# Kernel optimization log

Measured on AMD Instinct MI355X. Metric: run time of the kernel, lower is better.

The kernel has to match this reference:

```python
import jax, jax.numpy as jnp
import numpy as np
import math

N, D, F, G = 8192, 512, 2048, 102
GAMMA = 0.5
NEG = -1e9


def setup_inputs() -> dict:
    key = jax.random.key(0)
    ks = jax.random.split(key, 32)
    x = jax.random.normal(ks[0], (N, D), dtype=jnp.float32)
    real_edge_mask = jax.random.bernoulli(ks[1], 0.9, (N, N))  # True = masked (non-edge)
    fake_edge_mask = jax.random.bernoulli(ks[2], 0.1, (N, N))
    # per-row distinct sorted drop indices over gene_list = arange(D)
    r = jax.random.uniform(ks[3], (N, D))
    drop_idx = jnp.sort(jnp.argsort(r, axis=1)[:, :G], axis=1).astype(jnp.int32)
    s = 1.0 / math.sqrt(D)
    def W(k, m, n):
        return jax.random.normal(k, (m, n), dtype=jnp.float32) * s
    inp = {
        'x': x, 'drop_idx': drop_idx,
        'real_edge_mask': real_edge_mask, 'fake_edge_mask': fake_edge_mask,
        'enc_Wq_r': W(ks[4], D, D), 'enc_Wk_r': W(ks[5], D, D),
        'enc_Wq_f': W(ks[6], D, D), 'enc_Wk_f': W(ks[7], D, D), 'enc_Wv': W(ks[8], D, D),
        'dec_Wq_r': W(ks[9], D, D), 'dec_Wk_r': W(ks[10], D, D),
        'dec_Wq_f': W(ks[11], D, D), 'dec_Wk_f': W(ks[12], D, D), 'dec_Wv': W(ks[13], D, D),
        'ff_W1': W(ks[14], D, F), 'ff_b1': jnp.zeros((F,), jnp.float32),
        'ff_W2': W(ks[15], F, D), 'ff_b2': jnp.zeros((D,), jnp.float32),
        'ln1_g': jnp.ones((D,), jnp.float32), 'ln1_b': jnp.zeros((D,), jnp.float32),
        'ln2_g': jnp.ones((D,), jnp.float32), 'ln2_b': jnp.zeros((D,), jnp.float32),
        'ln3_g': jnp.ones((D,), jnp.float32), 'ln3_b': jnp.zeros((D,), jnp.float32),
        'head_W': W(ks[16], D, D), 'head_b': jnp.zeros((D,), jnp.float32),
    }
    return inp


def layer_norm(h, g, b, eps=1e-5):
    mu = h.mean(-1, keepdims=True)
    var = ((h - mu) ** 2).mean(-1, keepdims=True)
    return (h - mu) * jax.lax.rsqrt(var + eps) * g + b


def spatial_attention(h, Wq_r, Wk_r, Wq_f, Wk_f, Wv, rmask, fmask, gamma):
    d = h.shape[-1]
    scale = 1.0 / math.sqrt(d)
    sr = jnp.where(rmask, NEG, (h @ Wq_r) @ (h @ Wk_r).T * scale)  # [N,N]
    sf = jnp.where(fmask, NEG, (h @ Wq_f) @ (h @ Wk_f).T * scale)  # [N,N]
    m = jnp.maximum(sr.max(axis=1, keepdims=True), sf.max(axis=1, keepdims=True))
    scores = (jnp.exp(sr - m) + gamma * jnp.exp(sf - m)) / (1.0 + gamma)
    attn = scores / scores.sum(axis=-1, keepdims=True)
    return attn @ (h @ Wv), attn


def reference(x, drop_idx, real_edge_mask, fake_edge_mask,
              enc_Wq_r, enc_Wk_r, enc_Wq_f, enc_Wk_f, enc_Wv,
              dec_Wq_r, dec_Wk_r, dec_Wq_f, dec_Wk_f, dec_Wv,
              ff_W1, ff_b1, ff_W2, ff_b2,
              ln1_g, ln1_b, ln2_g, ln2_b, ln3_g, ln3_b,
              head_W, head_b):
    rows = jnp.arange(x.shape[0])[:, None]
    drop_x = x.at[rows, drop_idx].set(0.0)
    hidden, _ = spatial_attention(drop_x, enc_Wq_r, enc_Wk_r, enc_Wq_f, enc_Wk_f, enc_Wv,
                                  real_edge_mask, fake_edge_mask, GAMMA)
    hidden = layer_norm(hidden + drop_x, ln1_g, ln1_b)
    ff = jax.nn.gelu(hidden @ ff_W1 + ff_b1, approximate=False) @ ff_W2 + ff_b2
    hidden = layer_norm(hidden + ff, ln2_g, ln2_b)
    recon, _ = spatial_attention(hidden, dec_Wq_r, dec_Wk_r, dec_Wq_f, dec_Wk_f, dec_Wv,
                                 real_edge_mask, fake_edge_mask, GAMMA)
    recon = layer_norm(recon + hidden, ln3_g, ln3_b)
    h = recon @ head_W + head_b
    x_init = jnp.take_along_axis(x, drop_idx, axis=1)    # [N,G]
    x_recon = jnp.take_along_axis(h, drop_idx, axis=1)   # [N,G]
    return x_init, x_recon
```

## Files before the change

### kernel.cpp

```cpp
#include <hip/hip_runtime.h>
#include <cstdint>
#include <cstddef>


typedef unsigned short u16;
typedef __bf16 bf16x8 __attribute__((ext_vector_type(8)));
typedef float f32x4 __attribute__((ext_vector_type(4)));

#define GAMMA_C 0.5f
#define SCALE_C 0.04419417382415922f
#define NG      (8192 * 102)
#define SLAB    ((size_t)8192 * 512)

__device__ __forceinline__ float b2f(u16 u) {
  union { unsigned int i; float f; } c; c.i = ((unsigned int)u) << 16; return c.f;
}
__device__ __forceinline__ u16 f2b(float f) {
  union { float f; unsigned int i; } c; c.f = f;
  unsigned int u = c.i + 0x7FFFu + ((c.i >> 16) & 1u);
  return (u16)(u >> 16);
}
__device__ __forceinline__ float gelu_exact(float x) {
  return 0.5f * x * (1.0f + erff(x * 0.70710678118654752f));
}
__device__ __forceinline__ int idx_at(const void* p, int i, int i64) {
  return i64 ? (int)((const long long*)p)[i] : ((const int*)p)[i];
}
__device__ __forceinline__ float fl_at(const void* p, size_t i, int f32m) {
  return f32m ? ((const float*)p)[i] : b2f(((const u16*)p)[i]);
}
__device__ __forceinline__ void mask8(const void* m, size_t base, int f, bool o[8]) {
  if (f == 1) {
    unsigned long long v = *(const unsigned long long*)((const unsigned char*)m + base);
#pragma unroll
    for (int e = 0; e < 8; ++e) o[e] = ((v >> (8 * e)) & 0xFF) != 0;
  } else if (f == 0) {
    const uint4 a = *(const uint4*)((const int*)m + base);
    const uint4 b = *(const uint4*)((const int*)m + base + 4);
    o[0] = a.x; o[1] = a.y; o[2] = a.z; o[3] = a.w;
    o[4] = b.x; o[5] = b.y; o[6] = b.z; o[7] = b.w;
  } else if (f == 2) {
    const uint4 v = *(const uint4*)((const u16*)m + base);
    const u16* p = (const u16*)&v;
#pragma unroll
    for (int e = 0; e < 8; ++e) o[e] = p[e] != 0;
  } else {
    const uint4 a = *(const uint4*)((const float*)m + base);
    const uint4 b = *(const uint4*)((const float*)m + base + 4);
    o[0] = a.x; o[1] = a.y; o[2] = a.z; o[3] = a.w;
    o[4] = b.x; o[5] = b.y; o[6] = b.z; o[7] = b.w;
  }
}

#define GLD16(g, l) __builtin_amdgcn_global_load_lds(                         \
    (const __attribute__((address_space(1))) void*)(g),                       \
    (__attribute__((address_space(3))) void*)(l), 16, 0, 0)

__global__ void detect_all(const unsigned char* __restrict__ rmask,
                           const void* __restrict__ xin,
                           const void* __restrict__ idx,
                           int* __restrict__ flags) {
  __shared__ int nz[4];
  __shared__ int mx, bl;
  const int t = threadIdx.x;
  if (t < 4) nz[t] = 0;
  if (t == 0) { mx = 0; bl = 0; }
  __syncthreads();
  int cnt = 0, lm = 0;
  for (int i = t; i < 4096; i += 256) {
    const int v = rmask[i];
    if (v) { ++cnt; if (v > lm) lm = v; }
  }
  if (cnt) atomicAdd(&nz[t & 3], cnt);
  if (lm) atomicMax(&mx, lm);
  int bcnt = 0;
  for (int i = t; i < 2048; i += 256) {
    const u16 u = ((const u16*)xin)[2 * i];
    const int e = (u >> 7) & 0xFF;
    if ((e >= 110 && e <= 141) || u == 0) ++bcnt;
  }
  atomicAdd(&bl, bcnt);
  __syncthreads();
  if (t == 0) {
    int f;
    if (nz[1] == 0 && nz[2] == 0 && nz[3] == 0) f = 0;
    else if (nz[0] == 0 && nz[1] == 0) f = 3;
    else if (mx <= 1) f = 1;
    else f = 2;
    flags[0] = f;
    flags[2] = (bl >= 1536) ? 0 : 1;
    int ok = 1, prev = -1;
    for (int j = 0; j < 102; ++j) {
      const int v = ((const int*)idx)[j];
      if (v <= prev || v < 0 || v >= 512) { ok = 0; break; }
      prev = v;
    }
    flags[1] = ok ? 0 : 1;
  }
}

__global__ void bitmask_prep(const void* __restrict__ mr, const void* __restrict__ mf,
                             unsigned char* __restrict__ bmr, unsigned char* __restrict__ bmf,
                             const int* __restrict__ flags) {
  const int i = blockIdx.x * 256 + threadIdx.x;
  const int f = flags[0];
  bool mk[8];
  mask8(mr, (size_t)i * 8, f, mk);
  unsigned char b = 0;
#pragma unroll
  for (int e = 0; e < 8; ++e) b |= (unsigned char)mk[e] << e;
  bmr[i] = b;
  mask8(mf, (size_t)i * 8, f, mk);
  b = 0;
#pragma unroll
  for (int e = 0; e < 8; ++e) b |= (unsigned char)mk[e] << e;
  bmf[i] = b;
}

struct PtrPack { const void* p[11]; };
__global__ void transpose_cvt_b(PtrPack srcs, u16* __restrict__ out,
                                const int* __restrict__ flags) {
  __shared__ u16 tile[32][33];
  const void* in = srcs.p[blockIdx.z];
  u16* o = out + (size_t)blockIdx.z * 512 * 512;
  const int f32m = flags[2];
  const int c0 = blockIdx.x * 32, r0 = blockIdx.y * 32;
  const int tx = threadIdx.x, ty = threadIdx.y;
  for (int i = ty; i < 32; i += 8) {
    const size_t src = (size_t)(r0 + i) * 512 + (c0 + tx);
    tile[i][tx] = f32m ? f2b(((const float*)in)[src]) : ((const u16*)in)[src];
  }
  __syncthreads();
  for (int i = ty; i < 32; i += 8)
    o[(size_t)(c0 + i) * 512 + (r0 + tx)] = tile[tx][i];
}
__global__ void transpose_cvt(const void* __restrict__ in, u16* __restrict__ out,
                              int R, int C, const int* __restrict__ flags) {
  __shared__ u16 tile[32][33];
  const int f32m = flags[2];
  const int c0 = blockIdx.x * 32, r0 = blockIdx.y * 32;
  const int tx = threadIdx.x, ty = threadIdx.y;
  for (int i = ty; i < 32; i += 8) {
    const size_t src = (size_t)(r0 + i) * C + (c0 + tx);
    tile[i][tx] = f32m ? f2b(((const float*)in)[src]) : ((const u16*)in)[src];
  }
  __syncthreads();
  for (int i = ty; i < 32; i += 8)
    out[(size_t)(c0 + i) * R + (r0 + tx)] = tile[tx][i];
}

__global__ void cvt_to_bf16(const void* __restrict__ in, u16* __restrict__ out,
                            int n, const int* __restrict__ flags) {
  const int i = blockIdx.x * blockDim.x + threadIdx.x;
  if (i < n)
    out[i] = flags[2] ? f2b(((const float*)in)[i]) : ((const u16*)in)[i];
}
__global__ void zero_f32(float* __restrict__ p, int n) {
  const int i = blockIdx.x * blockDim.x + threadIdx.x;
  if (i < n) p[i] = 0.f;
}
__global__ void zero_drop(u16* __restrict__ dx, const void* __restrict__ idx,
                          const int* __restrict__ flags) {
  const int i = blockIdx.x * blockDim.x + threadIdx.x;
  if (i < NG) {
    const int row = i / 102;
    dx[(size_t)row * 512 + idx_at(idx, i, flags[1])] = 0;
  }
}
__global__ void gather_out_k(const void* __restrict__ x, const u16* __restrict__ hs,
                             const void* __restrict__ hb,
                             const void* __restrict__ idx, void* __restrict__ out,
                             const int* __restrict__ flags) {
  const int i = blockIdx.x * blockDim.x + threadIdx.x;
  if (i < NG) {
    const int row = i / 102;
    const int c = idx_at(idx, i, flags[1]);
    const size_t src = (size_t)row * 512 + c;
    const float hv = b2f(hs[src]) + b2f(hs[src + SLAB]) + fl_at(hb, c, flags[2]);
    if (flags[2]) {
      ((float*)out)[i] = ((const float*)x)[src];
      ((float*)out)[NG + i] = hv;
    } else {
      ((u16*)out)[i] = ((const u16*)x)[src];
      ((u16*)out)[NG + i] = f2b(hv);
    }
  }
}

__global__ __launch_bounds__(256)
void gemm_bt(const u16* __restrict__ A, int lda,
             const u16* __restrict__ Bt, int ldb,
             u16* __restrict__ C, int ldc,
             int K, int mode, const void* __restrict__ bias,
             const int* __restrict__ flags, u16* __restrict__ aux,
             long long slabStride) {
  __shared__ alignas(16) u16 smem[16384];
  u16* As = smem;
  u16* Bs = smem + 8192;
  const int tid = threadIdx.x;
  const int lane = tid & 63, wave = tid >> 6;
  const int l15 = lane & 15, l4 = lane >> 4;
  const int wm = (wave >> 1) << 6, wn = (wave & 1) << 6;
  const int m0 = blockIdx.y << 7, n0 = blockIdx.x << 7;
  const size_t kShift = (size_t)blockIdx.z * (size_t)K;
  C += (size_t)blockIdx.z * (size_t)slabStride;

  f32x4 acc[4][4];
#pragma unroll
  for (int i = 0; i < 4; ++i)
#pragma unroll
    for (int j = 0; j < 4; ++j) acc[i][j] = (f32x4){0.f, 0.f, 0.f, 0.f};

  const int lrow = lane >> 3;
  const int lcg = (lane & 7) ^ lrow;
  const u16* aG = A + kShift + (size_t)(m0 + wave * 8 + lrow) * lda + lcg * 8;
  const u16* bG = Bt + kShift + (size_t)(n0 + wave * 8 + lrow) * ldb + lcg * 8;
  u16* asDst = &As[(wave * 8) * 64];
  u16* bsDst = &Bs[(wave * 8) * 64];
  const int swz = (l15 & 7) << 3;

  for (int k0 = 0; k0 < K; k0 += 64) {
#pragma unroll
    for (int r = 0; r < 4; ++r) {
      GLD16(aG + (size_t)(r * 32) * lda + k0, asDst + r * 32 * 64);
      GLD16(bG + (size_t)(r * 32) * ldb + k0, bsDst + r * 32 * 64);
    }
    __syncthreads();
#pragma unroll
    for (int kk = 0; kk < 2; ++kk) {
      bf16x8 a[4], b[4];
      const int koff = (((kk << 2) + l4) << 3) ^ swz;
#pragma unroll
      for (int i = 0; i < 4; ++i) {
        a[i] = *(const bf16x8*)&As[(wm + (i << 4) + l15) * 64 + koff];
        b[i] = *(const bf16x8*)&Bs[(wn + (i << 4) + l15) * 64 + koff];
      }
#pragma unroll
      for (int i = 0; i < 4; ++i)
#pragma unroll
        for (int j = 0; j < 4; ++j)
          acc[i][j] = __builtin_amdgcn_mfma_f32_16x16x32_bf16(a[i], b[j], acc[i][j], 0, 0, 0);
    }
    __syncthreads();
  }

  const int f32m = flags[2];

  if (mode == 2 && n0 >= 2048) {
#pragma unroll
    for (int i = 0; i < 4; ++i) {
      const int rbase = m0 + wm + (i << 4) + l4 * 4;
#pragma unroll
      for (int j = 0; j < 4; ++j) {
        const int gn = n0 - 2048 + wn + (j << 4) + l15;
        ushort4 pk;
        pk.x = f2b(acc[i][j][0]); pk.y = f2b(acc[i][j][1]);
        pk.z = f2b(acc[i][j][2]); pk.w = f2b(acc[i][j][3]);
        *(ushort4*)&aux[(size_t)gn * 8192 + rbase] = pk;
      }
    }
    return;
  }

#pragma unroll
  for (int i = 0; i < 4; ++i) {
    const int rl0 = wm + (i << 4) + l4 * 4;
#pragma unroll
    for (int j = 0; j < 4; ++j) {
      const int cl = wn + (j << 4) + l15;
      float bv = 0.f;
      if (bias) bv = fl_at(bias, n0 + cl, f32m);
      const int chunk = cl >> 3, within = cl & 7;
#pragma unroll
      for (int r = 0; r < 4; ++r) {
        const int rl = rl0 + r;
        float v = acc[i][j][r] + bv;
        if (mode == 1) v = gelu_exact(v);
        const int wchunk = (chunk & 8) | ((chunk ^ rl) & 7);
        smem[rl * 128 + wchunk * 8 + within] = f2b(v);
      }
    }
  }
  __syncthreads();

  const int r = tid >> 1, h = tid & 1;
  const int grow = m0 + r;
#pragma unroll
  for (int cb = 0; cb < 8; ++cb) {
    const int chunkidx = h * 8 + cb;
    const int rchunk = (chunkidx & 8) | ((chunkidx ^ r) & 7);
    uint4 raw = *(const uint4*)&smem[r * 128 + rchunk * 8];
    *(uint4*)&C[(size_t)grow * ldc + n0 + chunkidx * 8] = raw;
  }
}

__global__ __launch_bounds__(256, 3)
void score_fused(const u16* __restrict__ P,
                 const unsigned char* __restrict__ bmr,
                 const unsigned char* __restrict__ bmf,
                 u16* __restrict__ W, float* __restrict__ lvec) {
  __shared__ alignas(16) u16 stage[16384];
  __shared__ unsigned long long mrs[256], mfs[256];
  const int tid = threadIdx.x;
  const int lane = tid & 63, wave = tid >> 6;
  const int l15 = lane & 15, l4 = lane >> 4;
  const int wm = (wave >> 1) << 6, wn = (wave & 1) << 6;
  const int m0 = blockIdx.y << 7, n0 = blockIdx.x << 7;

  {
    const int r = tid >> 1, hh = tid & 1;
    const size_t mo = (size_t)(m0 + r) * 1024 + (n0 >> 3) + hh * 8;
    mrs[tid] = *(const unsigned long long*)&bmr[mo];
    mfs[tid] = *(const unsigned long long*)&bmf[mo];
  }

  const int lrow = lane >> 3;
  const int lcg = (lane & 7) ^ lrow;
  const int swz = (l15 & 7) << 3;
  u16* asDst = &stage[(wave * 8) * 64];
  u16* bsDst = &stage[8192 + (wave * 8) * 64];

  unsigned int srp[4][4][2];
  f32x4 acc[4][4];

  for (int p = 0; p < 2; ++p) {
#pragma unroll
    for (int i = 0; i < 4; ++i)
#pragma unroll
      for (int j = 0; j < 4; ++j) acc[i][j] = (f32x4){0.f, 0.f, 0.f, 0.f};

    const u16* aG = P + (p ? 1024 : 0) + (size_t)(m0 + wave * 8 + lrow) * 2048 + lcg * 8;
    const u16* bG = P + (p ? 1536 : 512) + (size_t)(n0 + wave * 8 + lrow) * 2048 + lcg * 8;

    for (int k0 = 0; k0 < 512; k0 += 64) {
#pragma unroll
      for (int r = 0; r < 4; ++r) {
        GLD16(aG + (size_t)(r * 32) * 2048 + k0, asDst + r * 32 * 64);
        GLD16(bG + (size_t)(r * 32) * 2048 + k0, bsDst + r * 32 * 64);
      }
      __syncthreads();
#pragma unroll
      for (int kk = 0; kk < 2; ++kk) {
        bf16x8 a[4], b[4];
        const int koff = (((kk << 2) + l4) << 3) ^ swz;
#pragma unroll
        for (int i = 0; i < 4; ++i) {
          a[i] = *(const bf16x8*)&stage[(wm + (i << 4) + l15) * 64 + koff];
          b[i] = *(const bf16x8*)&stage[8192 + (wn + (i << 4) + l15) * 64 + koff];
        }
#pragma unroll
        for (int i = 0; i < 4; ++i)
#pragma unroll
          for (int j = 0; j < 4; ++j)
            acc[i][j] = __builtin_amdgcn_mfma_f32_16x16x32_bf16(a[i], b[j], acc[i][j], 0, 0, 0);
      }
      __syncthreads();
    }

    if (p == 0) {
#pragma unroll
      for (int i = 0; i < 4; ++i)
#pragma unroll
        for (int j = 0; j < 4; ++j) {
          srp[i][j][0] = (unsigned int)f2b(acc[i][j][0] * SCALE_C)
                       | ((unsigned int)f2b(acc[i][j][1] * SCALE_C) << 16);
          srp[i][j][1] = (unsigned int)f2b(acc[i][j][2] * SCALE_C)
                       | ((unsigned int)f2b(acc[i][j][3] * SCALE_C) << 16);
        }
    }
  }

  const int hb = wn >> 6;
#pragma unroll
  for (int i = 0; i < 4; ++i) {
    const int rl0 = wm + (i << 4) + l4 * 4;
#pragma unroll
    for (int r = 0; r < 4; ++r) {
      const int rl = rl0 + r;
      const unsigned long long mr = mrs[rl * 2 + hb];
      const unsigned long long mf = mfs[rl * 2 + hb];
      float rsum = 0.f;
#pragma unroll
      for (int j = 0; j < 4; ++j) {
        const int cl = wn + (j << 4) + l15;
        const int bit = cl & 63;
        const float srv = b2f((u16)(srp[i][j][r >> 1] >> ((r & 1) * 16)));
        const float sfv = acc[i][j][r] * SCALE_C;
        const float wr = ((mr >> bit) & 1) ? 0.f : __expf(srv);
        const float wf = ((mf >> bit) & 1) ? 0.f : __expf(sfv);
        const float w = wr + GAMMA_C * wf;
        rsum += w;
        const int chunk = cl >> 3, within = cl & 7;
        const int wchunk = (chunk & 8) | ((chunk ^ rl) & 7);
        stage[rl * 128 + wchunk * 8 + within] = f2b(w);
      }
      rsum += __shfl_xor(rsum, 1);
      rsum += __shfl_xor(rsum, 2);
      rsum += __shfl_xor(rsum, 4);
      rsum += __shfl_xor(rsum, 8);
      if (l15 == 0) atomicAdd(&lvec[m0 + rl], rsum);
    }
  }
  __syncthreads();

  const int rr = tid >> 1, hh = tid & 1;
  const int grow = m0 + rr;
#pragma unroll
  for (int cb = 0; cb < 8; ++cb) {
    const int chunkidx = hh * 8 + cb;
    const int rchunk = (chunkidx & 8) | ((chunkidx ^ rr) & 7);
    uint4 raw = *(const uint4*)&stage[rr * 128 + rchunk * 8];
    *(uint4*)&W[(size_t)grow * 8192 + n0 + chunkidx * 8] = raw;
  }
}

__global__ __launch_bounds__(512)
void pv_big(const u16* __restrict__ W, const u16* __restrict__ Vt,
            u16* __restrict__ slabs) {
  __shared__ alignas(16) u16 smem[24576];
  u16* As = smem;
  u16* Bs = smem + 8192;
  const int tid = threadIdx.x;
  const int lane = tid & 63, wave = tid >> 6;
  const int l15 = lane & 15, l4 = lane >> 4;
  const int wm = (wave >> 2) << 6;
  const int wn = (wave & 3) << 6;
  const int m0 = blockIdx.y << 7, n0 = blockIdx.x << 8;
  const int kbase = blockIdx.z << 10;
  u16* slab = slabs + (size_t)blockIdx.z * SLAB;

  f32x4 acc[4][4];
#pragma unroll
  for (int i = 0; i < 4; ++i)
#pragma unroll
    for (int j = 0; j < 4; ++j) acc[i][j] = (f32x4){0.f, 0.f, 0.f, 0.f};

  const int lrow = lane >> 3;
  const int lcg = (lane & 7) ^ lrow;
  const u16* aG = W + (size_t)(m0 + wave * 8 + lrow) * 8192 + kbase + lcg * 8;
  const u16* bG = Vt + (size_t)(n0 + wave * 8 + lrow) * 8192 + kbase + lcg * 8;
  u16* asDst = &As[(wave * 8) * 64];
  u16* bsDst = &Bs[(wave * 8) * 64];
  const int swz = (l15 & 7) << 3;

  for (int k0 = 0; k0 < 1024; k0 += 64) {
#pragma unroll
    for (int r = 0; r < 2; ++r)
      GLD16(aG + (size_t)(r * 64) * 8192 + k0, asDst + r * 64 * 64);
#pragma unroll
    for (int r = 0; r < 4; ++r)
      GLD16(bG + (size_t)(r * 64) * 8192 + k0, bsDst + r * 64 * 64);
    __syncthreads();
#pragma unroll
    for (int kk = 0; kk < 2; ++kk) {
      bf16x8 a[4], b[4];
      const int koff = (((kk << 2) + l4) << 3) ^ swz;
#pragma unroll
      for (int i = 0; i < 4; ++i) {
        a[i] = *(const bf16x8*)&As[(wm + (i << 4) + l15) * 64 + koff];
        b[i] = *(const bf16x8*)&Bs[(wn + (i << 4) + l15) * 64 + koff];
      }
#pragma unroll
      for (int i = 0; i < 4; ++i)
#pragma unroll
        for (int j = 0; j < 4; ++j)
          acc[i][j] = __builtin_amdgcn_mfma_f32_16x16x32_bf16(a[i], b[j], acc[i][j], 0, 0, 0);
    }
    __syncthreads();
  }

#pragma unroll
  for (int i = 0; i < 4; ++i) {
    const int rbase = m0 + wm + (i << 4) + l4 * 4;
#pragma unroll
    for (int j = 0; j < 4; ++j) {
      const int gn = n0 + wn + (j << 4) + l15;
      ushort4 pk;
      pk.x = f2b(acc[i][j][0]); pk.y = f2b(acc[i][j][1]);
      pk.z = f2b(acc[i][j][2]); pk.w = f2b(acc[i][j][3]);
      *(ushort4*)&slab[((size_t)(rbase >> 2) * 512 + gn) * 4] = pk;
    }
  }
}

__global__ __launch_bounds__(512)
void pv_ln4(const u16* __restrict__ slabs, const float* __restrict__ lvec,
            const u16* __restrict__ res, const void* __restrict__ g,
            const void* __restrict__ be, u16* __restrict__ out,
            const int* __restrict__ flags) {
  const int gid = blockIdx.x;
  const int col = threadIdx.x;
  const int lane = col & 63, wave = col >> 6;
  const int f32m = flags[2];
  float o[4] = {0.f, 0.f, 0.f, 0.f};
  const size_t base = ((size_t)gid * 512 + col) * 4;
#pragma unroll
  for (int s = 0; s < 8; ++s) {
    const ushort4 v = *(const ushort4*)&slabs[s * SLAB + base];
    o[0] += b2f(v.x); o[1] += b2f(v.y); o[2] += b2f(v.z); o[3] += b2f(v.w);
  }
  float v[4];
#pragma unroll
  for (int q = 0; q < 4; ++q) {
    const int grow = gid * 4 + q;
    v[q] = o[q] / lvec[grow] + b2f(res[(size_t)grow * 512 + col]);
  }
  __shared__ float s1[4][8], s2[4][8];
#pragma unroll
  for (int q = 0; q < 4; ++q) {
    float sm = v[q], sq = v[q] * v[q];
#pragma unroll
    for (int d = 1; d < 64; d <<= 1) {
      sm += __shfl_xor(sm, d);
      sq += __shfl_xor(sq, d);
    }
    if (lane == 0) { s1[q][wave] = sm; s2[q][wave] = sq; }
  }
  __syncthreads();
  const float gv = fl_at(g, col, f32m), bv = fl_at(be, col, f32m);
#pragma unroll
  for (int q = 0; q < 4; ++q) {
    float sm = 0.f, sq = 0.f;
#pragma unroll
    for (int w = 0; w < 8; ++w) { sm += s1[q][w]; sq += s2[q][w]; }
    const float mu = sm * (1.f / 512.f);
    const float var = sq * (1.f / 512.f) - mu * mu;
    const float rs = rsqrtf(var + 1e-5f);
    out[(size_t)(gid * 4 + q) * 512 + col] = f2b((v[q] - mu) * rs * gv + bv);
  }
}

__global__ __launch_bounds__(256)
void ff_ln(const u16* __restrict__ slabs, const void* __restrict__ bias,
           const u16* __restrict__ res, const void* __restrict__ g,
           const void* __restrict__ be, u16* __restrict__ out,
           const int* __restrict__ flags) {
  const int row = blockIdx.x, tid = threadIdx.x;
  const int f32m = flags[2];
  const size_t off = (size_t)row * 512 + tid * 2;
  const float v0 = b2f(slabs[off]) + b2f(slabs[off + SLAB])
                 + fl_at(bias, tid * 2, f32m) + b2f(res[off]);
  const float v1 = b2f(slabs[off + 1]) + b2f(slabs[off + 1 + SLAB])
                 + fl_at(bias, tid * 2 + 1, f32m) + b2f(res[off + 1]);
  __shared__ float r1[256], r2[256];
  r1[tid] = v0 + v1;
  r2[tid] = v0 * v0 + v1 * v1;
  __syncthreads();
  for (int s = 128; s > 0; s >>= 1) {
    if (tid < s) { r1[tid] += r1[tid + s]; r2[tid] += r2[tid + s]; }
    __syncthreads();
  }
  const float mu = r1[0] * (1.f / 512.f);
  const float var = r2[0] * (1.f / 512.f) - mu * mu;
  const float rs = rsqrtf(var + 1e-5f);
  out[off]     = f2b((v0 - mu) * rs * fl_at(g, tid * 2, f32m)     + fl_at(be, tid * 2, f32m));
  out[off + 1] = f2b((v1 - mu) * rs * fl_at(g, tid * 2 + 1, f32m) + fl_at(be, tid * 2 + 1, f32m));
}

extern "C" void kernel_launch(void* const* d_in, const int* in_sizes, int n_in,
                              void* d_out, int out_size, void* d_ws, size_t ws_size,
                              hipStream_t stream) {
  (void)in_sizes; (void)n_in; (void)out_size; (void)ws_size;
  const void* x = d_in[0];
  const void* dropidx = d_in[1];
  const void* rmask = d_in[2];
  const void* fmask = d_in[3];

  char* base = (char*)d_ws;
  size_t cur = 0;
  auto alloc = [&](size_t b) -> void* {
    void* p = base + cur;
    cur += (b + 255) & ~(size_t)255;
    return p;
  };

  int* flags = (int*)alloc(256);
  u16* Wt = (u16*)alloc((size_t)11 * 512 * 512 * 2);
  u16* wff1t = (u16*)alloc((size_t)2048 * 512 * 2);
  u16* wff2t = (u16*)alloc((size_t)512 * 2048 * 2);
  const size_t ND2 = (size_t)8192 * 512 * 2;
  u16* dropx = (u16*)alloc(ND2);
  u16* P = (u16*)alloc((size_t)8192 * 2048 * 2);
  u16* Vt = (u16*)alloc(ND2);
  u16* H1 = (u16*)alloc(ND2);
  u16* H2 = (u16*)alloc(ND2);
  u16* FF1 = (u16*)alloc((size_t)8192 * 2048 * 2);
  unsigned char* bmr = (unsigned char*)alloc((size_t)8192 * 1024);
  unsigned char* bmf = (unsigned char*)alloc((size_t)8192 * 1024);
  float* lvec = (float*)alloc((size_t)8192 * 4);
  u16* slabs = (u16*)alloc((size_t)8 * SLAB * 2);
  u16* Wb = (u16*)alloc((size_t)8192 * 8192 * 2);

  detect_all<<<1, 256, 0, stream>>>((const unsigned char*)rmask, x, dropidx, flags);
  bitmask_prep<<<32768, 256, 0, stream>>>(rmask, fmask, bmr, bmf, flags);

  const dim3 tb(32, 8);
  PtrPack wp;
  for (int i = 0; i < 5; ++i) wp.p[i] = d_in[4 + i];
  for (int i = 0; i < 5; ++i) wp.p[5 + i] = d_in[9 + i];
  wp.p[10] = d_in[24];
  transpose_cvt_b<<<dim3(16, 16, 11), tb, 0, stream>>>(wp, Wt, flags);
  transpose_cvt<<<dim3(64, 16), tb, 0, stream>>>(d_in[14], wff1t, 512, 2048, flags);
  transpose_cvt<<<dim3(16, 64), tb, 0, stream>>>(d_in[16], wff2t, 2048, 512, flags);

  cvt_to_bf16<<<(8192 * 512 + 255) / 256, 256, 0, stream>>>(x, dropx, 8192 * 512, flags);
  zero_drop<<<(NG + 255) / 256, 256, 0, stream>>>(dropx, dropidx, flags);

  auto gemm = [&](const u16* A, int lda, const u16* Bt, int ldb, u16* Cc, int ldc,
                  int M, int Nn, int K, int mode, const void* bias, u16* aux,
                  int zc, long long slabStride) {
    gemm_bt<<<dim3(Nn / 128, M / 128, zc), 256, 0, stream>>>(
        A, lda, Bt, ldb, Cc, ldc, K, mode, bias, flags, aux, slabStride);
  };

  auto attention = [&](const u16* Hin, const u16* Wqkv, const void* lnG,
                       const void* lnB, u16* outLN) {
    zero_f32<<<32, 256, 0, stream>>>(lvec, 8192);
    gemm(Hin, 512, Wqkv, 512, P, 2048, 8192, 2560, 512, 2, nullptr, Vt, 1, 0);
    score_fused<<<dim3(64, 64), 256, 0, stream>>>(P, bmr, bmf, Wb, lvec);
    pv_big<<<dim3(2, 64, 8), 512, 0, stream>>>(Wb, Vt, slabs);
    pv_ln4<<<2048, 512, 0, stream>>>(slabs, lvec, Hin, lnG, lnB, outLN, flags);
  };

  attention(dropx, Wt, d_in[18], d_in[19], H1);
  gemm(H1, 512, wff1t, 512, FF1, 2048, 8192, 2048, 512, 1, d_in[15], nullptr, 1, 0);
  gemm(FF1, 2048, wff2t, 2048, slabs, 512, 8192, 512, 1024, 0, nullptr, nullptr,
       2, (long long)SLAB);
  ff_ln<<<8192, 256, 0, stream>>>(slabs, d_in[17], H1, d_in[20], d_in[21], H2, flags);
  attention(H2, Wt + (size_t)5 * 512 * 512, d_in[22], d_in[23], H1);
  gemm(H1, 512, Wt + (size_t)10 * 512 * 512, 512, slabs, 512, 8192, 512, 256, 0,
       nullptr, nullptr, 2, (long long)SLAB);
  gather_out_k<<<(NG + 255) / 256, 256, 0, stream>>>(x, slabs, d_in[25], dropidx,
                                                     d_out, flags);
}
```

Baseline: 1.446 ms.

## Widen score tile to 128x256 with 512 threads and halve PV split-K

After: 1.506 ms. 1.04x slower.

```diff
diff --git a/kernel.cpp b/kernel.cpp
--- a/kernel.cpp
+++ b/kernel.cpp
@@ -294,24 +294,25 @@
   }
 }
 
-__global__ __launch_bounds__(256, 3)
+__global__ __launch_bounds__(512, 4)
 void score_fused(const u16* __restrict__ P,
                  const unsigned char* __restrict__ bmr,
                  const unsigned char* __restrict__ bmf,
                  u16* __restrict__ W, float* __restrict__ lvec) {
-  __shared__ alignas(16) u16 stage[16384];
-  __shared__ unsigned long long mrs[256], mfs[256];
+  __shared__ alignas(16) u16 stage[32768];
+  __shared__ unsigned long long mrs[128][4], mfs[128][4];
   const int tid = threadIdx.x;
   const int lane = tid & 63, wave = tid >> 6;
   const int l15 = lane & 15, l4 = lane >> 4;
-  const int wm = (wave >> 1) << 6, wn = (wave & 1) << 6;
-  const int m0 = blockIdx.y << 7, n0 = blockIdx.x << 7;
+  const int wm = (wave >> 2) << 6;
+  const int wn = (wave & 3) << 6;
+  const int m0 = blockIdx.y << 7, n0 = blockIdx.x << 8;
 
   {
-    const int r = tid >> 1, hh = tid & 1;
-    const size_t mo = (size_t)(m0 + r) * 1024 + (n0 >> 3) + hh * 8;
-    mrs[tid] = *(const unsigned long long*)&bmr[mo];
-    mfs[tid] = *(const unsigned long long*)&bmf[mo];
+    const int rl = tid >> 2, q = tid & 3;
+    const size_t mo = (size_t)(m0 + rl) * 1024 + (n0 >> 3) + q * 8;
+    mrs[rl][q] = *(const unsigned long long*)&bmr[mo];
+    mfs[rl][q] = *(const unsigned long long*)&bmf[mo];
   }
 
   const int lrow = lane >> 3;
@@ -334,10 +335,11 @@
 
     for (int k0 = 0; k0 < 512; k0 += 64) {
 #pragma unroll
-      for (int r = 0; r < 4; ++r) {
-        GLD16(aG + (size_t)(r * 32) * 2048 + k0, asDst + r * 32 * 64);
-        GLD16(bG + (size_t)(r * 32) * 2048 + k0, bsDst + r * 32 * 64);
-      }
+      for (int r = 0; r < 2; ++r)
+        GLD16(aG + (size_t)(r * 64) * 2048 + k0, asDst + r * 64 * 64);
+#pragma unroll
+      for (int r = 0; r < 4; ++r)
+        GLD16(bG + (size_t)(r * 64) * 2048 + k0, bsDst + r * 64 * 64);
       __syncthreads();
 #pragma unroll
       for (int kk = 0; kk < 2; ++kk) {
@@ -370,29 +372,29 @@
     }
   }
 
-  const int hb = wn >> 6;
+  const int qw = wn >> 6;
 #pragma unroll
   for (int i = 0; i < 4; ++i) {
     const int rl0 = wm + (i << 4) + l4 * 4;
 #pragma unroll
     for (int r = 0; r < 4; ++r) {
       const int rl = rl0 + r;
-      const unsigned long long mr = mrs[rl * 2 + hb];
-      const unsigned long long mf = mfs[rl * 2 + hb];
+      const unsigned long long mr = mrs[rl][qw];
+      const unsigned long long mf = mfs[rl][qw];
       float rsum = 0.f;
 #pragma unroll
       for (int j = 0; j < 4; ++j) {
-        const int cl = wn + (j << 4) + l15;
-        const int bit = cl & 63;
+        const int bit = (j << 4) + l15;
         const float srv = b2f((u16)(srp[i][j][r >> 1] >> ((r & 1) * 16)));
         const float sfv = acc[i][j][r] * SCALE_C;
         const float wr = ((mr >> bit) & 1) ? 0.f : __expf(srv);
         const float wf = ((mf >> bit) & 1) ? 0.f : __expf(sfv);
         const float w = wr + GAMMA_C * wf;
         rsum += w;
+        const int cl = wn + (j << 4) + l15;
         const int chunk = cl >> 3, within = cl & 7;
-        const int wchunk = (chunk & 8) | ((chunk ^ rl) & 7);
-        stage[rl * 128 + wchunk * 8 + within] = f2b(w);
+        const int wchunk = (chunk & 24) | ((chunk ^ rl) & 7);
+        stage[rl * 256 + wchunk * 8 + within] = f2b(w);
       }
       rsum += __shfl_xor(rsum, 1);
       rsum += __shfl_xor(rsum, 2);
@@ -403,14 +405,14 @@
   }
   __syncthreads();
 
-  const int rr = tid >> 1, hh = tid & 1;
+  const int rr = tid >> 2, qq = tid & 3;
   const int grow = m0 + rr;
 #pragma unroll
   for (int cb = 0; cb < 8; ++cb) {
-    const int chunkidx = hh * 8 + cb;
-    const int rchunk = (chunkidx & 8) | ((chunkidx ^ rr) & 7);
-    uint4 raw = *(const uint4*)&stage[rr * 128 + rchunk * 8];
-    *(uint4*)&W[(size_t)grow * 8192 + n0 + chunkidx * 8] = raw;
+    const int chunk = qq * 8 + cb;
+    const int rchunk = (chunk & 24) | ((chunk ^ rr) & 7);
+    uint4 raw = *(const uint4*)&stage[rr * 256 + rchunk * 8];
+    *(uint4*)&W[(size_t)grow * 8192 + n0 + chunk * 8] = raw;
   }
 }
 
@@ -426,7 +428,7 @@
   const int wm = (wave >> 2) << 6;
   const int wn = (wave & 3) << 6;
   const int m0 = blockIdx.y << 7, n0 = blockIdx.x << 8;
-  const int kbase = blockIdx.z << 10;
+  const int kbase = blockIdx.z << 11;
   u16* slab = slabs + (size_t)blockIdx.z * SLAB;
 
   f32x4 acc[4][4];
@@ -443,7 +445,7 @@
   u16* bsDst = &Bs[(wave * 8) * 64];
   const int swz = (l15 & 7) << 3;
 
-  for (int k0 = 0; k0 < 1024; k0 += 64) {
+  for (int k0 = 0; k0 < 2048; k0 += 64) {
 #pragma unroll
     for (int r = 0; r < 2; ++r)
       GLD16(aG + (size_t)(r * 64) * 8192 + k0, asDst + r * 64 * 64);
@@ -495,7 +497,7 @@
   float o[4] = {0.f, 0.f, 0.f, 0.f};
   const size_t base = ((size_t)gid * 512 + col) * 4;
 #pragma unroll
-  for (int s = 0; s < 8; ++s) {
+  for (int s = 0; s < 4; ++s) {
     const ushort4 v = *(const ushort4*)&slabs[s * SLAB + base];
     o[0] += b2f(v.x); o[1] += b2f(v.y); o[2] += b2f(v.z); o[3] += b2f(v.w);
   }
@@ -588,7 +590,7 @@
   unsigned char* bmr = (unsigned char*)alloc((size_t)8192 * 1024);
   unsigned char* bmf = (unsigned char*)alloc((size_t)8192 * 1024);
   float* lvec = (float*)alloc((size_t)8192 * 4);
-  u16* slabs = (u16*)alloc((size_t)8 * SLAB * 2);
+  u16* slabs = (u16*)alloc((size_t)4 * SLAB * 2);
   u16* Wb = (u16*)alloc((size_t)8192 * 8192 * 2);
 
   detect_all<<<1, 256, 0, stream>>>((const unsigned char*)rmask, x, dropidx, flags);
@@ -617,8 +619,8 @@
                        const void* lnB, u16* outLN) {
     zero_f32<<<32, 256, 0, stream>>>(lvec, 8192);
     gemm(Hin, 512, Wqkv, 512, P, 2048, 8192, 2560, 512, 2, nullptr, Vt, 1, 0);
-    score_fused<<<dim3(64, 64), 256, 0, stream>>>(P, bmr, bmf, Wb, lvec);
-    pv_big<<<dim3(2, 64, 8), 512, 0, stream>>>(Wb, Vt, slabs);
+    score_fused<<<dim3(32, 64), 512, 0, stream>>>(P, bmr, bmf, Wb, lvec);
+    pv_big<<<dim3(2, 64, 4), 512, 0, stream>>>(Wb, Vt, slabs);
     pv_ln4<<<2048, 512, 0, stream>>>(slabs, lvec, Hin, lnG, lnB, outLN, flags);
   };
 
```
